# Kernel tuning notes

Hardware: AMD Instinct MI355X
Metric: run time of the kernel (lower is better)

The kernel has to match this reference:

```python
import jax, jax.numpy as jnp
import numpy as np

B, F, V, D = 4096, 8, 1000, 1024  # batch, n_fields, vocab per field, hidden_size
LN_EPS = 1e-5


def layer_norm(x, g, b, eps=LN_EPS):
    mu = x.mean(axis=-1, keepdims=True)
    var = ((x - mu) ** 2).mean(axis=-1, keepdims=True)
    return (x - mu) * jax.lax.rsqrt(var + eps) * g + b


def setup_inputs() -> dict:
    key = jax.random.key(0)
    k0, k1, k2, k3 = jax.random.split(key, 4)
    return {
        "input_embedding": jax.random.normal(k0, (B, D), jnp.float32),
        "features": jax.random.randint(k1, (B, F), 0, V),
        "embed_tables": jax.random.normal(k2, (F, V, D), jnp.float32) * 0.02,
        "ln_gamma": jnp.ones((D,), jnp.float32),
        "ln_beta": jnp.zeros((D,), jnp.float32),
        "pred_W": jax.random.normal(k3, (F, D, V), jnpp := jnp.float32) * 0.02,
        "pred_b": jnp.zeros((F, V), jnp.float32),
    }


def reference(input_embedding, features, embed_tables, ln_gamma, ln_beta, pred_W, pred_b):
    # Per-field embedding lookup: (B, F, D)
    feat_emb = embed_tables[jnp.arange(F)[None, :], features]
    # Stack input embedding first, as in torch.stack([input_embedding] + ...):
    embeddings = jnp.concatenate([input_embedding[:, None, :], feat_emb], axis=1)  # (B, F+1, D)
    # triu(diagonal=1) masked broadcast-sum then [:, 1:, :] == exclusive causal prefix sum:
    # masked_sums[:, j] = sum_{i < j+1} embeddings[:, i] for j = 0..F-1
    masked_sums = jnp.cumsum(embeddings, axis=1)[:, :F, :]  # (B, F, D)
    h = jax.nn.gelu(layer_norm(masked_sums, ln_gamma, ln_beta), approximate=False)
    # Per-field predictor heads (Linear(D, V)), batched over fields:
    logits = jnp.einsum("bfd,fdv->bfv", h, pred_W) + pred_b  # (B, F, V)
    return logits
```

## Files before the change

kernel.cpp:

```cpp
#include <hip/hip_runtime.h>
#include <hip/hip_bf16.h>

#define B_ 4096
#define F_ 8
#define V_ 1000
#define D_ 1024
#define VP 1024

typedef __bf16 bf16x8 __attribute__((ext_vector_type(8)));
typedef float f32x4 __attribute__((ext_vector_type(4)));

__device__ __forceinline__ void gload_lds16(const void* g, void* l) {
  __builtin_amdgcn_global_load_lds(
      (const __attribute__((address_space(1))) void*)g,
      (__attribute__((address_space(3))) void*)l, 16, 0, 0);
}

__device__ __forceinline__ void phase_barrier() {
  __builtin_amdgcn_sched_barrier(0);
  __builtin_amdgcn_s_barrier();
  __builtin_amdgcn_sched_barrier(0);
}

__global__ __launch_bounds__(256) void transpose_w(
    const float* __restrict__ W, __hip_bfloat16* __restrict__ Wt) {
  __shared__ float tile[32][33];
  const int f = blockIdx.z;
  const int k0 = blockIdx.x * 32;
  const int v0 = blockIdx.y * 32;
  const int tx = threadIdx.x;
  const int ty = threadIdx.y;
  const float* Wf = W + (size_t)f * D_ * V_;
#pragma unroll
  for (int i = 0; i < 4; ++i) {
    int k = k0 + ty + i * 8;
    int v = v0 + tx;
    tile[ty + i * 8][tx] = (v < V_) ? Wf[k * V_ + v] : 0.0f;
  }
  __syncthreads();
  __hip_bfloat16* Wtf = Wt + (size_t)f * VP * D_;
#pragma unroll
  for (int i = 0; i < 4; ++i) {
    int v = v0 + ty + i * 8;
    int k = k0 + tx;
    Wtf[v * D_ + k] = __float2bfloat16(tile[tx][ty + i * 8]);
  }
}

__global__ __launch_bounds__(256) void fuse_h(
    const float* __restrict__ emb, const int* __restrict__ feats,
    const float* __restrict__ tables, const float* __restrict__ gamma,
    const float* __restrict__ beta, __hip_bfloat16* __restrict__ H) {
  const int b = blockIdx.x;
  const int t = threadIdx.x;
  const int d = t * 4;
  const int wave = t >> 6, lane = t & 63;

  float s[4];
  {
    float4 v = *reinterpret_cast<const float4*>(&emb[(size_t)b * D_ + d]);
    s[0] = v.x; s[1] = v.y; s[2] = v.z; s[3] = v.w;
  }
  float gm[4], bt[4];
  {
    float4 g = *reinterpret_cast<const float4*>(&gamma[d]);
    float4 bb = *reinterpret_cast<const float4*>(&beta[d]);
    gm[0] = g.x; gm[1] = g.y; gm[2] = g.z; gm[3] = g.w;
    bt[0] = bb.x; bt[1] = bb.y; bt[2] = bb.z; bt[3] = bb.w;
  }
  __shared__ float red[4][2];

  for (int f = 0; f < F_; ++f) {
    float sum = s[0] + s[1] + s[2] + s[3];
    float ssq = s[0] * s[0] + s[1] * s[1] + s[2] * s[2] + s[3] * s[3];
#pragma unroll
    for (int off = 32; off > 0; off >>= 1) {
      sum += __shfl_xor(sum, off, 64);
      ssq += __shfl_xor(ssq, off, 64);
    }
    if (lane == 0) { red[wave][0] = sum; red[wave][1] = ssq; }
    __syncthreads();
    sum = red[0][0] + red[1][0] + red[2][0] + red[3][0];
    ssq = red[0][1] + red[1][1] + red[2][1] + red[3][1];
    __syncthreads();

    const float mu = sum * (1.0f / D_);
    const float var = ssq * (1.0f / D_) - mu * mu;
    const float rstd = rsqrtf(var + 1e-5f);

    __hip_bfloat16 hb[4];
#pragma unroll
    for (int j = 0; j < 4; ++j) {
      float x = (s[j] - mu) * rstd * gm[j] + bt[j];
      float g = 0.5f * x * (1.0f + erff(x * 0.70710678118654752f));
      hb[j] = __float2bfloat16(g);
    }
    *reinterpret_cast<uint2*>(&H[(size_t)f * (B_ * D_) + (size_t)b * D_ + d]) =
        *reinterpret_cast<const uint2*>(hb);

    if (f < F_ - 1) {
      int feat = feats[b * F_ + f];
      const float* row = tables + ((size_t)f * V_ + feat) * D_;
      float4 tv = *reinterpret_cast<const float4*>(&row[d]);
      s[0] += tv.x; s[1] += tv.y; s[2] += tv.z; s[3] += tv.w;
    }
  }
}

#define AOFF 0
#define BOFF 32768

#define STAGE(OPB, GB, DBUF, HALF, KT)                                        \
  do {                                                                        \
    const ushort* _g = (GB) + (size_t)(HALF) * (128 * D_) + (size_t)(KT) * 64;\
    ushort* _l = &lds[(OPB) + ((DBUF)*2 + (HALF)) * 8192 + w * 512];          \
    gload_lds16(_g, _l);                                                      \
    gload_lds16(_g + 64 * D_, _l + 4096);                                     \
  } while (0)

#define LD_A(DST, LBASE, FIOFF)                                               \
  _Pragma("unroll") for (int _fj = 0; _fj < 4; ++_fj)                         \
  _Pragma("unroll") for (int _ks = 0; _ks < 2; ++_ks)                         \
      DST[_fj][_ks] = *reinterpret_cast<const bf16x8*>(                       \
          (LBASE) + ((((FIOFF) + _fj) * 2 + _ks) * 512));

#define LD_B(DST, LBASE, NFOFF)                                               \
  _Pragma("unroll") for (int _fn = 0; _fn < 2; ++_fn)                         \
  _Pragma("unroll") for (int _ks = 0; _ks < 2; ++_ks)                         \
      DST[_fn][_ks] = *reinterpret_cast<const bf16x8*>(                       \
          (LBASE) + ((((NFOFF) + _fn) * 2 + _ks) * 512));

#define Q_MFMA(AF, BF, R0, C0)                                                \
  do {                                                                        \
    __builtin_amdgcn_s_setprio(1);                                            \
    _Pragma("unroll") for (int _fj = 0; _fj < 4; ++_fj)                       \
    _Pragma("unroll") for (int _fn = 0; _fn < 2; ++_fn)                       \
    _Pragma("unroll") for (int _ks = 0; _ks < 2; ++_ks)                       \
        acc[(R0) + _fj][(C0) + _fn] =                                         \
            __builtin_amdgcn_mfma_f32_16x16x32_bf16(                          \
                AF[_fj][_ks], BF[_fn][_ks], acc[(R0) + _fj][(C0) + _fn],      \
                0, 0, 0);                                                     \
    __builtin_amdgcn_s_setprio(0);                                            \
  } while (0)

#define WAITV4 asm volatile("s_waitcnt vmcnt(4)" ::: "memory")
#define WAITV0 asm volatile("s_waitcnt vmcnt(0)" ::: "memory")

__global__ __launch_bounds__(512, 2) void gemm_hw(
    const ushort* __restrict__ H,
    const ushort* __restrict__ Wt,
    const float* __restrict__ bias,
    float* __restrict__ out) {
  __shared__ ushort lds[65536];

  const int bid = blockIdx.x;
  const int swz = (bid & 7) * 64 + (bid >> 3);
  const int f = swz >> 6;
  const int r = swz & 63;
  const int mt = r >> 2, nt = r & 3;

  const int t = threadIdx.x;
  const int w = t >> 6, l = t & 63;
  const int wm = w >> 2;
  const int wn = w & 3;

  const ushort* Hf = H + (size_t)f * (B_ * D_);
  const ushort* Wf = Wt + (size_t)f * (VP * D_);

  const int srow = ((w >> 1) << 4) + (l >> 2);
  const int skx = ((w & 1) << 5) + ((((l & 3) << 3)) ^ (((l >> 5) & 1) << 4));
  const ushort* gA = Hf + (size_t)(mt * 256 + srow) * D_ + skx;
  const ushort* gB = Wf + (size_t)(nt * 256 + srow) * D_ + skx;

  const int laneu =
      ((l & 15) << 5) + (((((l >> 4) << 4)) ^ (((l >> 3) & 1) << 5)) >> 1);
  const ushort* lA[2] = {&lds[(0 * 2 + wm) * 8192 + laneu],
                         &lds[(1 * 2 + wm) * 8192 + laneu]};
  const ushort* lB[2] = {
      &lds[BOFF + (0 * 2 + (wn >> 1)) * 8192 + (wn & 1) * 4096 + laneu],
      &lds[BOFF + (1 * 2 + (wn >> 1)) * 8192 + (wn & 1) * 4096 + laneu]};

  bf16x8 a0[4][2], a1[4][2], b0[2][2], b1[2][2];
  f32x4 acc[8][4] = {};

  STAGE(AOFF, gA, 0, 0, 0);
  STAGE(AOFF, gA, 0, 1, 0);
  STAGE(BOFF, gB, 0, 0, 0);
  STAGE(BOFF, gB, 0, 1, 0);
  STAGE(AOFF, gA, 1, 0, 1);
  STAGE(AOFF, gA, 1, 1, 1);
  WAITV4;
  phase_barrier();

#pragma unroll 1
  for (int i = 0; i < 8; ++i) {
    const int t1 = 2 * i + 1, t2 = 2 * i + 2, t3 = 2 * i + 3;
    const bool more = (i < 7);
    LD_A(a0, lA[0], 0);
    LD_B(b0, lB[0], 0);
    STAGE(BOFF, gB, 1, 0, t1);
    phase_barrier();
    Q_MFMA(a0, b0, 0, 0);
    phase_barrier();
    LD_A(a1, lA[0], 4);
    STAGE(BOFF, gB, 1, 1, t1);
    phase_barrier();
    Q_MFMA(a1, b0, 4, 0);
    phase_barrier();
    LD_B(b1, lB[0], 2);
    if (more) STAGE(AOFF, gA, 0, 0, t2);
    phase_barrier();
    Q_MFMA(a0, b1, 0, 2);
    phase_barrier();
    if (more) STAGE(AOFF, gA, 0, 1, t2);
    phase_barrier();
    Q_MFMA(a1, b1, 4, 2);
    if (more) { WAITV4; } else { WAITV0; }
    phase_barrier();
    LD_A(a0, lA[1], 0);
    LD_B(b0, lB[1], 0);
    if (more) STAGE(BOFF, gB, 0, 0, t2);
    phase_barrier();
    Q_MFMA(a0, b0, 0, 0);
    phase_barrier();
    LD_A(a1, lA[1], 4);
    if (more) STAGE(BOFF, gB, 0, 1, t2);
    phase_barrier();
    Q_MFMA(a1, b0, 4, 0);
    phase_barrier();
    LD_B(b1, lB[1], 2);
    if (more) STAGE(AOFF, gA, 1, 0, t3);
    phase_barrier();
    Q_MFMA(a0, b1, 0, 2);
    phase_barrier();
    if (more) STAGE(AOFF, gA, 1, 1, t3);
    phase_barrier();
    Q_MFMA(a1, b1, 4, 2);
    if (more) WAITV4;
    phase_barrier();
  }

  const float* bp = bias + f * V_;
  const int orow0 = mt * 256 + wm * 128 + ((l >> 4) << 2);
  const int ocol0 = nt * 256 + wn * 64 + (l & 15);
#pragma unroll
  for (int fi = 0; fi < 8; ++fi) {
#pragma unroll
    for (int fn = 0; fn < 4; ++fn) {
      int col = ocol0 + fn * 16;
      if (col < V_) {
        float bb = bp[col];
        int row = orow0 + fi * 16;
        float* op = out + (size_t)row * (F_ * V_) + (size_t)f * V_ + col;
#pragma unroll
        for (int q = 0; q < 4; ++q)
          op[(size_t)q * (F_ * V_)] = acc[fi][fn][q] + bb;
      }
    }
  }
}

extern "C" void kernel_launch(void* const* d_in, const int* in_sizes, int n_in,
                              void* d_out, int out_size, void* d_ws,
                              size_t ws_size, hipStream_t stream) {
  const float* emb = (const float*)d_in[0];
  const int* feats = (const int*)d_in[1];
  const float* tables = (const float*)d_in[2];
  const float* gamma = (const float*)d_in[3];
  const float* beta = (const float*)d_in[4];
  const float* W = (const float*)d_in[5];
  const float* bias = (const float*)d_in[6];
  float* out = (float*)d_out;

  char* ws = (char*)d_ws;
  __hip_bfloat16* Hbuf = (__hip_bfloat16*)ws;
  __hip_bfloat16* Wtbuf =
      (__hip_bfloat16*)(ws + (size_t)F_ * B_ * D_ * 2);

  transpose_w<<<dim3(D_ / 32, VP / 32, F_), dim3(32, 8), 0, stream>>>(W, Wtbuf);
  fuse_h<<<dim3(B_), dim3(256), 0, stream>>>(emb, feats, tables, gamma, beta,
                                             Hbuf);
  gemm_hw<<<dim3((B_ / 256) * (VP / 256) * F_), dim3(512), 0, stream>>>(
      (const ushort*)Hbuf, (const ushort*)Wtbuf, bias, out);
}
```

Baseline: 136.4 us.

## Halve barriers in GEMM main loop and deepen prefetch of B stage

Rewrites the pipelined bf16 GEMM main loop so each MFMA quarter is separated by a single workgroup barrier instead of two, and replaces sched_barrier fences with plain compiler memory clobbers. B-tile global-to-LDS loads are issued one slot earlier, with the vmcnt wait raised from 4 to 6 to keep more loads in flight. This cuts synchronisation overhead and lets the compiler interleave MFMAs with loads more freely. The cost is a tighter LDS buffer-reuse schedule that risks read/write races if the ordering is wrong.

```diff
diff --git a/kernel.cpp b/kernel.cpp
--- a/kernel.cpp
+++ b/kernel.cpp
@@ -14,12 +14,6 @@
   __builtin_amdgcn_global_load_lds(
       (const __attribute__((address_space(1))) void*)g,
       (__attribute__((address_space(3))) void*)l, 16, 0, 0);
-}
-
-__device__ __forceinline__ void phase_barrier() {
-  __builtin_amdgcn_sched_barrier(0);
-  __builtin_amdgcn_s_barrier();
-  __builtin_amdgcn_sched_barrier(0);
 }
 
 __global__ __launch_bounds__(256) void transpose_w(
@@ -143,7 +137,14 @@
     __builtin_amdgcn_s_setprio(0);                                            \
   } while (0)
 
-#define WAITV4 asm volatile("s_waitcnt vmcnt(4)" ::: "memory")
+#define PHB                                                                   \
+  do {                                                                        \
+    asm volatile("" ::: "memory");                                            \
+    __builtin_amdgcn_s_barrier();                                             \
+    asm volatile("" ::: "memory");                                            \
+  } while (0)
+
+#define WAITV6 asm volatile("s_waitcnt vmcnt(6)" ::: "memory")
 #define WAITV0 asm volatile("s_waitcnt vmcnt(0)" ::: "memory")
 
 __global__ __launch_bounds__(512, 2) void gemm_hw(
@@ -189,8 +190,9 @@
   STAGE(BOFF, gB, 0, 1, 0);
   STAGE(AOFF, gA, 1, 0, 1);
   STAGE(AOFF, gA, 1, 1, 1);
-  WAITV4;
-  phase_barrier();
+  STAGE(BOFF, gB, 1, 0, 1);
+  WAITV6;
+  PHB;
 
 #pragma unroll 1
   for (int i = 0; i < 8; ++i) {
@@ -198,46 +200,40 @@
     const bool more = (i < 7);
     LD_A(a0, lA[0], 0);
     LD_B(b0, lB[0], 0);
-    STAGE(BOFF, gB, 1, 0, t1);
-    phase_barrier();
+    STAGE(BOFF, gB, 1, 1, t1);
+    PHB;
     Q_MFMA(a0, b0, 0, 0);
-    phase_barrier();
     LD_A(a1, lA[0], 4);
-    STAGE(BOFF, gB, 1, 1, t1);
-    phase_barrier();
+    if (more) STAGE(AOFF, gA, 0, 0, t2);
+    PHB;
     Q_MFMA(a1, b0, 4, 0);
-    phase_barrier();
     LD_B(b1, lB[0], 2);
-    if (more) STAGE(AOFF, gA, 0, 0, t2);
-    phase_barrier();
+    if (more) STAGE(AOFF, gA, 0, 1, t2);
+    PHB;
     Q_MFMA(a0, b1, 0, 2);
-    phase_barrier();
-    if (more) STAGE(AOFF, gA, 0, 1, t2);
-    phase_barrier();
+    if (more) STAGE(BOFF, gB, 0, 0, t2);
+    if (more) { WAITV6; } else { WAITV0; }
+    PHB;
     Q_MFMA(a1, b1, 4, 2);
-    if (more) { WAITV4; } else { WAITV0; }
-    phase_barrier();
     LD_A(a0, lA[1], 0);
     LD_B(b0, lB[1], 0);
-    if (more) STAGE(BOFF, gB, 0, 0, t2);
-    phase_barrier();
+    if (more) STAGE(BOFF, gB, 0, 1, t2);
+    PHB;
     Q_MFMA(a0, b0, 0, 0);
-    phase_barrier();
     LD_A(a1, lA[1], 4);
-    if (more) STAGE(BOFF, gB, 0, 1, t2);
-    phase_barrier();
+    if (more) STAGE(AOFF, gA, 1, 0, t3);
+    PHB;
     Q_MFMA(a1, b0, 4, 0);
-    phase_barrier();
     LD_B(b1, lB[1], 2);
-    if (more) STAGE(AOFF, gA, 1, 0, t3);
-    phase_barrier();
+    if (more) STAGE(AOFF, gA, 1, 1, t3);
+    PHB;
     Q_MFMA(a0, b1, 0, 2);
-    phase_barrier();
-    if (more) STAGE(AOFF, gA, 1, 1, t3);
-    phase_barrier();
+    if (more) {
+      STAGE(BOFF, gB, 1, 0, t3);
+      WAITV6;
+    }
+    PHB;
     Q_MFMA(a1, b1, 4, 2);
-    if (more) WAITV4;
-    phase_barrier();
   }
 
   const float* bp = bias + f * V_;
```

New measurement: 135.8 us. Within noise of the previous version (-0.5%).
